# Performance work log

Measured on AMD Instinct MI355X. Metric: run time of the kernel, lower is better.

Reference implementation:

```python
import jax, jax.numpy as jnp
import numpy as np

HH, WW = 7, 7  # pooled output size (module init: height, width)


def setup_inputs() -> dict:
    key = jax.random.key(0)
    k1, k2, k3, k4, k5 = jax.random.split(key, 5)
    C, Hf, Wf = 512, 64, 256        # conv feature map (stride 8)
    B = 4096                        # number of RoI boxes
    img_h, img_w = 512, 2048        # original image size
    feats = jax.random.normal(k1, (C, Hf, Wf), dtype=jnp.float32)
    w = jax.random.uniform(k2, (B,), minval=16.0, maxval=256.0)
    h = jax.random.uniform(k3, (B,), minval=16.0, maxval=128.0)
    xc = jax.random.uniform(k4, (B,), minval=0.0, maxval=float(img_w))
    yc = jax.random.uniform(k5, (B,), minval=0.0, maxval=float(img_h))
    boxes = jnp.stack([xc, yc, w, h], axis=1).astype(jnp.float32)  # (B,4) xc,yc,w,h in image coords
    return {"feats": feats, "boxes": boxes, "img_height": img_h, "img_width": img_w}


def _bilinear_sample(feats, px, py):
    """feats: (C,Hf,Wf); px,py: (B,HH,WW) pixel coords in feature map. Zero padding outside."""
    C, Hf, Wf = feats.shape
    x0 = jnp.floor(px)
    y0 = jnp.floor(py)
    x1 = x0 + 1.0
    y1 = y0 + 1.0
    wx1 = px - x0
    wx0 = 1.0 - wx1
    wy1 = py - y0
    wy0 = 1.0 - wy1

    def gather(xi, yi):
        valid = (xi >= 0) & (xi <= Wf - 1) & (yi >= 0) & (yi <= Hf - 1)
        xi_c = jnp.clip(xi, 0, Wf - 1).astype(jnp.int32)
        yi_c = jnp.clip(yi, 0, Hf - 1).astype(jnp.int32)
        v = feats[:, yi_c, xi_c]                     # (C,B,HH,WW)
        return v * valid[None].astype(feats.dtype)

    out = (gather(x0, y0) * (wx0 * wy0)[None]
           + gather(x1, y0) * (wx1 * wy0)[None]
           + gather(x0, y1) * (wx0 * wy1)[None]
           + gather(x1, y1) * (wx1 * wy1)[None])    # (C,B,HH,WW)
    return jnp.transpose(out, (1, 0, 2, 3))          # (B,C,HH,WW)


def reference(feats, boxes, img_height, img_width):
    # box_to_affine (densecap BoxToAffine, align_corners=True normalization) fused
    # with affine_grid: sample coords computed inline per box.
    B = boxes.shape[0]
    C, Hf, Wf = feats.shape
    xc, yc, w, h = boxes[:, 0], boxes[:, 1], boxes[:, 2], boxes[:, 3]
    tx = jnp.linspace(-1.0, 1.0, WW, dtype=feats.dtype)
    ty = jnp.linspace(-1.0, 1.0, HH, dtype=feats.dtype)
    inv_w = 1.0 / (img_width - 1)
    inv_h = 1.0 / (img_height - 1)
    # normalized image coords: gx = (2*xc-(W-1))/(W-1) + tx * w/(W-1)
    gx = (2.0 * xc[:, None] - (img_width - 1)) * inv_w + (w * inv_w)[:, None] * tx[None, :]   # (B,WW)
    gy = (2.0 * yc[:, None] - (img_height - 1)) * inv_h + (h * inv_h)[:, None] * ty[None, :]  # (B,HH)
    # map normalized [-1,1] to feature-map pixel coords (align_corners=True)
    px = (gx + 1.0) * 0.5 * (Wf - 1)
    py = (gy + 1.0) * 0.5 * (Hf - 1)
    px = jnp.broadcast_to(px[:, None, :], (B, HH, WW))
    py = jnp.broadcast_to(py[:, :, None], (B, HH, WW))
    return _bilinear_sample(feats, px, py)            # (B,C,HH,WW)
```

## Files before the change

### kernel.cpp

```cpp
#include <hip/hip_runtime.h>
#include <math.h>

#define HH 7
#define WW 7
#define CC 512
#define HF 64
#define WF 256
#define NS 49
#define TILE_PAD 257

__global__ __launch_bounds__(256) void transpose_feats(const float* __restrict__ in,
                                                       float* __restrict__ out) {
    __shared__ float tile[32][33];
    const int P = HF * WF;
    int p  = blockIdx.x * 32 + threadIdx.x;
    int cb = blockIdx.y * 32;
#pragma unroll
    for (int r = 0; r < 32; r += 8)
        tile[threadIdx.y + r][threadIdx.x] = in[(size_t)(cb + threadIdx.y + r) * P + p];
    __syncthreads();
    int c  = cb + threadIdx.x;
    int pb = blockIdx.x * 32;
#pragma unroll
    for (int r = 0; r < 32; r += 8)
        out[(size_t)(pb + threadIdx.y + r) * CC + c] = tile[threadIdx.x][threadIdx.y + r];
}

__global__ __launch_bounds__(256) void roi_pool(const float* __restrict__ src,
                                                const float* __restrict__ boxes,
                                                const int* __restrict__ ih_p,
                                                const int* __restrict__ iw_p,
                                                float* __restrict__ out,
                                                int cellmul, int cmul) {
    __shared__ int4   s_off[NS];
    __shared__ float4 s_wt[NS];
    __shared__ float  tile[NS * TILE_PAD];

    const int b   = blockIdx.x;
    const int tid = threadIdx.x;

    if (tid < NS) {
        int i = tid / WW;
        int j = tid - i * WW;
        float IW1 = (float)(iw_p[0] - 1);
        float IH1 = (float)(ih_p[0] - 1);
        float xc = boxes[b * 4 + 0];
        float yc = boxes[b * 4 + 1];
        float bw = boxes[b * 4 + 2];
        float bh = boxes[b * 4 + 3];
        float inv_w = 1.0f / IW1;
        float inv_h = 1.0f / IH1;
        float tx = (float)(j - 3) * (1.0f / 3.0f);
        float ty = (float)(i - 3) * (1.0f / 3.0f);
        float gx = (2.0f * xc - IW1) * inv_w + (bw * inv_w) * tx;
        float gy = (2.0f * yc - IH1) * inv_h + (bh * inv_h) * ty;
        float px = (gx + 1.0f) * 0.5f * (float)(WF - 1);
        float py = (gy + 1.0f) * 0.5f * (float)(HF - 1);

        float x0f = floorf(px), y0f = floorf(py);
        float wx1 = px - x0f, wx0 = 1.0f - wx1;
        float wy1 = py - y0f, wy0 = 1.0f - wy1;
        float x1f = x0f + 1.0f, y1f = y0f + 1.0f;

        bool vx0 = (x0f >= 0.0f) && (x0f <= (float)(WF - 1));
        bool vx1 = (x1f >= 0.0f) && (x1f <= (float)(WF - 1));
        bool vy0 = (y0f >= 0.0f) && (y0f <= (float)(HF - 1));
        bool vy1 = (y1f >= 0.0f) && (y1f <= (float)(HF - 1));

        int xi0 = (int)fminf(fmaxf(x0f, 0.0f), (float)(WF - 1));
        int xi1 = (int)fminf(fmaxf(x1f, 0.0f), (float)(WF - 1));
        int yi0 = (int)fminf(fmaxf(y0f, 0.0f), (float)(HF - 1));
        int yi1 = (int)fminf(fmaxf(y1f, 0.0f), (float)(HF - 1));

        int4 o;
        o.x = (yi0 * WF + xi0) * cellmul;
        o.y = (yi0 * WF + xi1) * cellmul;
        o.z = (yi1 * WF + xi0) * cellmul;
        o.w = (yi1 * WF + xi1) * cellmul;
        float4 w4;
        w4.x = wx0 * wy0 * ((vx0 && vy0) ? 1.0f : 0.0f);
        w4.y = wx1 * wy0 * ((vx1 && vy0) ? 1.0f : 0.0f);
        w4.z = wx0 * wy1 * ((vx0 && vy1) ? 1.0f : 0.0f);
        w4.w = wx1 * wy1 * ((vx1 && vy1) ? 1.0f : 0.0f);
        s_off[tid] = o;
        s_wt[tid]  = w4;
    }
    __syncthreads();

    const size_t outbase = (size_t)b * (CC * NS);

    for (int c0 = 0; c0 < CC; c0 += 256) {
        const int cterm = (c0 + tid) * cmul;
#pragma unroll 7
        for (int s = 0; s < NS; ++s) {
            int4   o = s_off[s];
            float4 w = s_wt[s];
            float v = src[o.x + cterm] * w.x + src[o.y + cterm] * w.y +
                      src[o.z + cterm] * w.z + src[o.w + cterm] * w.w;
            tile[s * TILE_PAD + tid] = v;
        }
        __syncthreads();
        const size_t ob = outbase + (size_t)c0 * NS;
#pragma unroll
        for (int k = tid; k < 256 * NS; k += 256) {
            int cl = k / NS;
            int s  = k - cl * NS;
            out[ob + k] = tile[s * TILE_PAD + cl];
        }
        __syncthreads();
    }
}

extern "C" void kernel_launch(void* const* d_in, const int* in_sizes, int n_in,
                              void* d_out, int out_size, void* d_ws, size_t ws_size,
                              hipStream_t stream) {
    const float* feats = (const float*)d_in[0];
    const float* boxes = (const float*)d_in[1];
    const int*   ih    = (const int*)d_in[2];
    const int*   iw    = (const int*)d_in[3];
    float*       out   = (float*)d_out;
    const int B = in_sizes[1] / 4;

    const size_t need = (size_t)CC * HF * WF * sizeof(float);
    if (ws_size >= need) {
        float* tf = (float*)d_ws;
        dim3 tb(32, 8);
        dim3 tg((HF * WF) / 32, CC / 32);
        transpose_feats<<<tg, tb, 0, stream>>>(feats, tf);
        roi_pool<<<B, 256, 0, stream>>>(tf, boxes, ih, iw, out, CC, 1);
    } else {
        roi_pool<<<B, 256, 0, stream>>>(feats, boxes, ih, iw, out, 1, HF * WF);
    }
}
```

Baseline: 548.2 us.

## Vectorize RoI gather with float4 loads and nontemporal float4 output stores

The main RoI pool kernel now has each thread load four contiguous channels as float4 from the channel-last feature copy, with the four 64-thread groups splitting the 49 sample points. The output write-back packs four consecutive elements into a vector and uses nontemporal stores. Tile padding changes to 260 so float4 shared-memory writes stay aligned. The aim is fewer, wider memory transactions on both gather and store, at the cost of more index arithmetic and possible LDS bank conflicts on the scalar reads that pack the output vectors.

```diff
diff --git a/kernel.cpp b/kernel.cpp
--- a/kernel.cpp
+++ b/kernel.cpp
@@ -7,7 +7,10 @@
 #define HF 64
 #define WF 256
 #define NS 49
-#define TILE_PAD 257
+#define TILE_PAD 260
+#define NE4 ((256 * NS) / 4)
+
+typedef float floatv4 __attribute__((ext_vector_type(4)));
 
 __global__ __launch_bounds__(256) void transpose_feats(const float* __restrict__ in,
                                                        float* __restrict__ out) {
@@ -26,62 +29,75 @@
         out[(size_t)(pb + threadIdx.y + r) * CC + c] = tile[threadIdx.x][threadIdx.y + r];
 }
 
-__global__ __launch_bounds__(256) void roi_pool(const float* __restrict__ src,
-                                                const float* __restrict__ boxes,
-                                                const int* __restrict__ ih_p,
-                                                const int* __restrict__ iw_p,
-                                                float* __restrict__ out,
-                                                int cellmul, int cmul) {
+__device__ __forceinline__ void box_setup(int s, int b,
+                                          const float* __restrict__ boxes,
+                                          const int* __restrict__ ih_p,
+                                          const int* __restrict__ iw_p,
+                                          int4* o_out, float4* w_out) {
+    int i = s / WW;
+    int j = s - i * WW;
+    float IW1 = (float)(iw_p[0] - 1);
+    float IH1 = (float)(ih_p[0] - 1);
+    float xc = boxes[b * 4 + 0];
+    float yc = boxes[b * 4 + 1];
+    float bw = boxes[b * 4 + 2];
+    float bh = boxes[b * 4 + 3];
+    float inv_w = 1.0f / IW1;
+    float inv_h = 1.0f / IH1;
+    float tx = (float)(j - 3) * (1.0f / 3.0f);
+    float ty = (float)(i - 3) * (1.0f / 3.0f);
+    float gx = (2.0f * xc - IW1) * inv_w + (bw * inv_w) * tx;
+    float gy = (2.0f * yc - IH1) * inv_h + (bh * inv_h) * ty;
+    float px = (gx + 1.0f) * 0.5f * (float)(WF - 1);
+    float py = (gy + 1.0f) * 0.5f * (float)(HF - 1);
+
+    float x0f = floorf(px), y0f = floorf(py);
+    float wx1 = px - x0f, wx0 = 1.0f - wx1;
+    float wy1 = py - y0f, wy0 = 1.0f - wy1;
+    float x1f = x0f + 1.0f, y1f = y0f + 1.0f;
+
+    bool vx0 = (x0f >= 0.0f) && (x0f <= (float)(WF - 1));
+    bool vx1 = (x1f >= 0.0f) && (x1f <= (float)(WF - 1));
+    bool vy0 = (y0f >= 0.0f) && (y0f <= (float)(HF - 1));
+    bool vy1 = (y1f >= 0.0f) && (y1f <= (float)(HF - 1));
+
+    int xi0 = (int)fminf(fmaxf(x0f, 0.0f), (float)(WF - 1));
+    int xi1 = (int)fminf(fmaxf(x1f, 0.0f), (float)(WF - 1));
+    int yi0 = (int)fminf(fmaxf(y0f, 0.0f), (float)(HF - 1));
+    int yi1 = (int)fminf(fmaxf(y1f, 0.0f), (float)(HF - 1));
+
+    int4 o;
+    o.x = yi0 * WF + xi0;
+    o.y = yi0 * WF + xi1;
+    o.z = yi1 * WF + xi0;
+    o.w = yi1 * WF + xi1;
+    float4 w4;
+    w4.x = wx0 * wy0 * ((vx0 && vy0) ? 1.0f : 0.0f);
+    w4.y = wx1 * wy0 * ((vx1 && vy0) ? 1.0f : 0.0f);
+    w4.z = wx0 * wy1 * ((vx0 && vy1) ? 1.0f : 0.0f);
+    w4.w = wx1 * wy1 * ((vx1 && vy1) ? 1.0f : 0.0f);
+    *o_out = o;
+    *w_out = w4;
+}
+
+__global__ __launch_bounds__(256) void roi_pool_v2(const float* __restrict__ src,
+                                                   const float* __restrict__ boxes,
+                                                   const int* __restrict__ ih_p,
+                                                   const int* __restrict__ iw_p,
+                                                   float* __restrict__ out) {
     __shared__ int4   s_off[NS];
     __shared__ float4 s_wt[NS];
     __shared__ float  tile[NS * TILE_PAD];
 
     const int b   = blockIdx.x;
     const int tid = threadIdx.x;
+    const int g   = tid & 63;
+    const int sp  = tid >> 6;
 
     if (tid < NS) {
-        int i = tid / WW;
-        int j = tid - i * WW;
-        float IW1 = (float)(iw_p[0] - 1);
-        float IH1 = (float)(ih_p[0] - 1);
-        float xc = boxes[b * 4 + 0];
-        float yc = boxes[b * 4 + 1];
-        float bw = boxes[b * 4 + 2];
-        float bh = boxes[b * 4 + 3];
-        float inv_w = 1.0f / IW1;
-        float inv_h = 1.0f / IH1;
-        float tx = (float)(j - 3) * (1.0f / 3.0f);
-        float ty = (float)(i - 3) * (1.0f / 3.0f);
-        float gx = (2.0f * xc - IW1) * inv_w + (bw * inv_w) * tx;
-        float gy = (2.0f * yc - IH1) * inv_h + (bh * inv_h) * ty;
-        float px = (gx + 1.0f) * 0.5f * (float)(WF - 1);
-        float py = (gy + 1.0f) * 0.5f * (float)(HF - 1);
-
-        float x0f = floorf(px), y0f = floorf(py);
-        float wx1 = px - x0f, wx0 = 1.0f - wx1;
-        float wy1 = py - y0f, wy0 = 1.0f - wy1;
-        float x1f = x0f + 1.0f, y1f = y0f + 1.0f;
-
-        bool vx0 = (x0f >= 0.0f) && (x0f <= (float)(WF - 1));
-        bool vx1 = (x1f >= 0.0f) && (x1f <= (float)(WF - 1));
-        bool vy0 = (y0f >= 0.0f) && (y0f <= (float)(HF - 1));
-        bool vy1 = (y1f >= 0.0f) && (y1f <= (float)(HF - 1));
-
-        int xi0 = (int)fminf(fmaxf(x0f, 0.0f), (float)(WF - 1));
-        int xi1 = (int)fminf(fmaxf(x1f, 0.0f), (float)(WF - 1));
-        int yi0 = (int)fminf(fmaxf(y0f, 0.0f), (float)(HF - 1));
-        int yi1 = (int)fminf(fmaxf(y1f, 0.0f), (float)(HF - 1));
-
-        int4 o;
-        o.x = (yi0 * WF + xi0) * cellmul;
-        o.y = (yi0 * WF + xi1) * cellmul;
-        o.z = (yi1 * WF + xi0) * cellmul;
-        o.w = (yi1 * WF + xi1) * cellmul;
-        float4 w4;
-        w4.x = wx0 * wy0 * ((vx0 && vy0) ? 1.0f : 0.0f);
-        w4.y = wx1 * wy0 * ((vx1 && vy0) ? 1.0f : 0.0f);
-        w4.z = wx0 * wy1 * ((vx0 && vy1) ? 1.0f : 0.0f);
-        w4.w = wx1 * wy1 * ((vx1 && vy1) ? 1.0f : 0.0f);
+        int4 o; float4 w4;
+        box_setup(tid, b, boxes, ih_p, iw_p, &o, &w4);
+        o.x *= (CC / 4); o.y *= (CC / 4); o.z *= (CC / 4); o.w *= (CC / 4);
         s_off[tid] = o;
         s_wt[tid]  = w4;
     }
@@ -90,22 +106,78 @@
     const size_t outbase = (size_t)b * (CC * NS);
 
     for (int c0 = 0; c0 < CC; c0 += 256) {
-        const int cterm = (c0 + tid) * cmul;
-#pragma unroll 7
+        const float4* src4 = (const float4*)(src + c0);
+        for (int s = sp; s < NS; s += 4) {
+            int4   o = s_off[s];
+            float4 w = s_wt[s];
+            float4 a = src4[o.x + g];
+            float4 bb = src4[o.y + g];
+            float4 c = src4[o.z + g];
+            float4 d = src4[o.w + g];
+            float4 v;
+            v.x = a.x * w.x + bb.x * w.y + c.x * w.z + d.x * w.w;
+            v.y = a.y * w.x + bb.y * w.y + c.y * w.z + d.y * w.w;
+            v.z = a.z * w.x + bb.z * w.y + c.z * w.z + d.z * w.w;
+            v.w = a.w * w.x + bb.w * w.y + c.w * w.z + d.w * w.w;
+            *(float4*)(&tile[s * TILE_PAD + 4 * g]) = v;
+        }
+        __syncthreads();
+        float* outc = out + outbase + (size_t)c0 * NS;
+#pragma unroll 4
+        for (int k4 = tid; k4 < NE4; k4 += 256) {
+            int e = k4 * 4;
+            int c = e / NS;
+            int s = e - c * NS;
+            floatv4 v;
+            v.x = tile[s * TILE_PAD + c];
+            if (++s == NS) { s = 0; ++c; }
+            v.y = tile[s * TILE_PAD + c];
+            if (++s == NS) { s = 0; ++c; }
+            v.z = tile[s * TILE_PAD + c];
+            if (++s == NS) { s = 0; ++c; }
+            v.w = tile[s * TILE_PAD + c];
+            __builtin_nontemporal_store(v, (floatv4*)outc + k4);
+        }
+        __syncthreads();
+    }
+}
+
+__global__ __launch_bounds__(256) void roi_pool_fb(const float* __restrict__ src,
+                                                   const float* __restrict__ boxes,
+                                                   const int* __restrict__ ih_p,
+                                                   const int* __restrict__ iw_p,
+                                                   float* __restrict__ out) {
+    __shared__ int4   s_off[NS];
+    __shared__ float4 s_wt[NS];
+    __shared__ float  tile[NS * 257];
+
+    const int b   = blockIdx.x;
+    const int tid = threadIdx.x;
+
+    if (tid < NS) {
+        int4 o; float4 w4;
+        box_setup(tid, b, boxes, ih_p, iw_p, &o, &w4);
+        s_off[tid] = o;
+        s_wt[tid]  = w4;
+    }
+    __syncthreads();
+
+    const size_t outbase = (size_t)b * (CC * NS);
+    for (int c0 = 0; c0 < CC; c0 += 256) {
+        const int cterm = (c0 + tid) * (HF * WF);
         for (int s = 0; s < NS; ++s) {
             int4   o = s_off[s];
             float4 w = s_wt[s];
             float v = src[o.x + cterm] * w.x + src[o.y + cterm] * w.y +
                       src[o.z + cterm] * w.z + src[o.w + cterm] * w.w;
-            tile[s * TILE_PAD + tid] = v;
+            tile[s * 257 + tid] = v;
         }
         __syncthreads();
         const size_t ob = outbase + (size_t)c0 * NS;
-#pragma unroll
         for (int k = tid; k < 256 * NS; k += 256) {
             int cl = k / NS;
             int s  = k - cl * NS;
-            out[ob + k] = tile[s * TILE_PAD + cl];
+            out[ob + k] = tile[s * 257 + cl];
         }
         __syncthreads();
     }
@@ -127,8 +199,8 @@
         dim3 tb(32, 8);
         dim3 tg((HF * WF) / 32, CC / 32);
         transpose_feats<<<tg, tb, 0, stream>>>(feats, tf);
-        roi_pool<<<B, 256, 0, stream>>>(tf, boxes, ih, iw, out, CC, 1);
+        roi_pool_v2<<<B, 256, 0, stream>>>(tf, boxes, ih, iw, out);
     } else {
-        roi_pool<<<B, 256, 0, stream>>>(feats, boxes, ih, iw, out, 1, HF * WF);
-    }
-}
+        roi_pool_fb<<<B, 256, 0, stream>>>(feats, boxes, ih, iw, out);
+    }
+}
```

Result: faster. 536.8 us (-2.1%).
